# Performance work log

Hardware: AMD Instinct MI355X
Metric: run time of the kernel (lower is better)

The kernel has to match this reference:

```python
import jax, jax.numpy as jnp
import numpy as np

T, B, I, H, L = 512, 64, 1024, 1024, 2


def setup_inputs() -> dict:
    key = jax.random.key(0)
    ks = jax.random.split(key, 3)
    stdv = 1.0 / np.sqrt(H)
    x = jax.random.normal(ks[0], (T, B, I), dtype=jnp.float32)
    w_ih = jax.random.uniform(ks[1], (L, 4 * H, I), dtype=jnp.float32, minval=-stdv, maxval=stdv)
    w_hh = jax.random.uniform(ks[2], (L, 4 * H, H), dtype=jnp.float32, minval=-stdv, maxval=stdv)
    b_ih = jnp.zeros((L, 4 * H), dtype=jnp.float32)
    b_hh = jnp.zeros((L, 4 * H), dtype=jnp.float32)
    h0 = jnp.zeros((L, B, H), dtype=jnp.float32)
    c0 = jnp.zeros((L, B, H), dtype=jnp.float32)
    return {"x": x, "h0": h0, "c0": c0, "w_ih": w_ih, "w_hh": w_hh, "b_ih": b_ih, "b_hh": b_hh}


def _lstm_layer(seq, h, c, w_ih_l, w_hh_l, b_ih_l, b_hh_l):
    # in2hidden: one big GEMM over all timesteps, as in the torch code
    igates = jnp.einsum('tbi,gi->tbg', seq, w_ih_l) + b_ih_l  # (T, B, 4H)

    def step(carry, ig):
        h, c = carry
        gates = ig + h @ w_hh_l.T + b_hh_l          # (B, 4H)
        i_g, f_g, g_g, o_g = jnp.split(gates, 4, axis=-1)
        c = jax.nn.sigmoid(f_g) * c + jax.nn.sigmoid(i_g) * jnp.tanh(g_g)
        h = jax.nn.sigmoid(o_g) * jnp.tanh(c)
        return (h, c), h

    (hT, cT), out = jax.lax.scan(step, (h, c), igates)
    return out, hT, cT


def reference(x, h0, c0, w_ih, w_hh, b_ih, b_hh):
    out = x
    h_fin, c_fin = [], []
    for l in range(L):  # small fixed number of structurally distinct layers
        out, hT, cT = _lstm_layer(out, h0[l], c0[l], w_ih[l], w_hh[l], b_ih[l], b_hh[l])
        h_fin.append(hT)
        c_fin.append(cT)
    return out, jnp.stack(h_fin), jnp.stack(c_fin)
```

## Files before the change

### kernel.cpp

```cpp
#include <hip/hip_runtime.h>
#include <hip/hip_bf16.h>
#include <stdint.h>

#define T_STEPS 512
#define NBATCH 64
#define HID 1024
#define NGATE 4096
#define NLAYERS 2
#define BH (NBATCH * HID)
#define TBH (T_STEPS * NBATCH * HID)
#define WEL ((size_t)NLAYERS * NGATE * HID)
#define GBLK 128

typedef __attribute__((ext_vector_type(8))) short short8;
typedef __attribute__((ext_vector_type(4))) float f32x4;

__device__ __forceinline__ ushort f2bf(float f) {
  union { float f; uint32_t i; } u; u.f = f;
  return (ushort)((u.i + 0x7fffu + ((u.i >> 16) & 1u)) >> 16);
}
__device__ __forceinline__ void gll16(const void* g, void* l) {
  __builtin_amdgcn_global_load_lds(
      (const __attribute__((address_space(1))) unsigned int*)g,
      (__attribute__((address_space(3))) unsigned int*)l, 16, 0, 0);
}

#define ISSC(S, P, OFF) \
  asm volatile("global_load_dwordx4 %0, %1, off offset:" #OFF \
               : "=v"(fr[S]) : "v"(P));
#define VMW(N, SLOT) \
  asm volatile("s_waitcnt vmcnt(" #N ")" : "+v"(fr[SLOT]));
#define CON(SLOT, KC) { \
    const short8 b0v = *(const short8*)(bb0 + ((((KC) * 64) + kb) ^ bsw)); \
    const short8 b1v = *(const short8*)(bb1 + ((((KC) * 64) + kb) ^ bsw)); \
    accA = __builtin_amdgcn_mfma_f32_16x16x32_bf16(fr[SLOT], b0v, accA, 0, 0, 0); \
    accB = __builtin_amdgcn_mfma_f32_16x16x32_bf16(fr[SLOT], b1v, accB, 0, 0, 0); }

#define PIPE64() \
  ISSC(0,A0p,0)    ISSC(1,A0p,64)   ISSC(2,A0p,128)  ISSC(3,A0p,192)  \
  ISSC(4,A0p,256)  ISSC(5,A0p,320)  ISSC(6,A0p,384)  ISSC(7,A0p,448)  \
  ISSC(8,A0p,512)  ISSC(9,A0p,576)  ISSC(10,A0p,640) ISSC(11,A0p,704) \
  ISSC(12,A0p,768) ISSC(13,A0p,832) ISSC(14,A0p,896) ISSC(15,A0p,960) \
  VMW(15,0)  CON(0,0)   ISSC(0,A0p,1024)  \
  VMW(15,1)  CON(1,1)   ISSC(1,A0p,1088)  \
  VMW(15,2)  CON(2,2)   ISSC(2,A0p,1152)  \
  VMW(15,3)  CON(3,3)   ISSC(3,A0p,1216)  \
  VMW(15,4)  CON(4,4)   ISSC(4,A0p,1280)  \
  VMW(15,5)  CON(5,5)   ISSC(5,A0p,1344)  \
  VMW(15,6)  CON(6,6)   ISSC(6,A0p,1408)  \
  VMW(15,7)  CON(7,7)   ISSC(7,A0p,1472)  \
  VMW(15,8)  CON(8,8)   ISSC(8,A0p,1536)  \
  VMW(15,9)  CON(9,9)   ISSC(9,A0p,1600)  \
  VMW(15,10) CON(10,10) ISSC(10,A0p,1664) \
  VMW(15,11) CON(11,11) ISSC(11,A0p,1728) \
  VMW(15,12) CON(12,12) ISSC(12,A0p,1792) \
  VMW(15,13) CON(13,13) ISSC(13,A0p,1856) \
  VMW(15,14) CON(14,14) ISSC(14,A0p,1920) \
  VMW(15,15) CON(15,15) ISSC(15,A0p,1984) \
  VMW(15,0)  CON(0,16)  ISSC(0,A1p,0)     \
  VMW(15,1)  CON(1,17)  ISSC(1,A1p,64)    \
  VMW(15,2)  CON(2,18)  ISSC(2,A1p,128)   \
  VMW(15,3)  CON(3,19)  ISSC(3,A1p,192)   \
  VMW(15,4)  CON(4,20)  ISSC(4,A1p,256)   \
  VMW(15,5)  CON(5,21)  ISSC(5,A1p,320)   \
  VMW(15,6)  CON(6,22)  ISSC(6,A1p,384)   \
  VMW(15,7)  CON(7,23)  ISSC(7,A1p,448)   \
  VMW(15,8)  CON(8,24)  ISSC(8,A1p,512)   \
  VMW(15,9)  CON(9,25)  ISSC(9,A1p,576)   \
  VMW(15,10) CON(10,26) ISSC(10,A1p,640)  \
  VMW(15,11) CON(11,27) ISSC(11,A1p,704)  \
  VMW(15,12) CON(12,28) ISSC(12,A1p,768)  \
  VMW(15,13) CON(13,29) ISSC(13,A1p,832)  \
  VMW(15,14) CON(14,30) ISSC(14,A1p,896)  \
  VMW(15,15) CON(15,31) ISSC(15,A1p,960)  \
  VMW(15,0)  CON(0,32)  ISSC(0,A1p,1024)  \
  VMW(15,1)  CON(1,33)  ISSC(1,A1p,1088)  \
  VMW(15,2)  CON(2,34)  ISSC(2,A1p,1152)  \
  VMW(15,3)  CON(3,35)  ISSC(3,A1p,1216)  \
  VMW(15,4)  CON(4,36)  ISSC(4,A1p,1280)  \
  VMW(15,5)  CON(5,37)  ISSC(5,A1p,1344)  \
  VMW(15,6)  CON(6,38)  ISSC(6,A1p,1408)  \
  VMW(15,7)  CON(7,39)  ISSC(7,A1p,1472)  \
  VMW(15,8)  CON(8,40)  ISSC(8,A1p,1536)  \
  VMW(15,9)  CON(9,41)  ISSC(9,A1p,1600)  \
  VMW(15,10) CON(10,42) ISSC(10,A1p,1664) \
  VMW(15,11) CON(11,43) ISSC(11,A1p,1728) \
  VMW(15,12) CON(12,44) ISSC(12,A1p,1792) \
  VMW(15,13) CON(13,45) ISSC(13,A1p,1856) \
  VMW(15,14) CON(14,46) ISSC(14,A1p,1920) \
  VMW(15,15) CON(15,47) ISSC(15,A1p,1984) \
  VMW(15,0)  CON(0,48)  \
  VMW(14,1)  CON(1,49)  \
  VMW(13,2)  CON(2,50)  \
  VMW(12,3)  CON(3,51)  \
  VMW(11,4)  CON(4,52)  \
  VMW(10,5)  CON(5,53)  \
  VMW(9,6)   CON(6,54)  \
  VMW(8,7)   CON(7,55)  \
  VMW(7,8)   CON(8,56)  \
  VMW(6,9)   CON(9,57)  \
  VMW(5,10)  CON(10,58) \
  VMW(4,11)  CON(11,59) \
  VMW(3,12)  CON(12,60) \
  VMW(2,13)  CON(13,61) \
  VMW(1,14)  CON(14,62) \
  VMW(0,15)  CON(15,63)

__global__ void k_f32_to_bf16(const float* __restrict__ in, ushort* __restrict__ out, int n) {
  int i = (blockIdx.x * blockDim.x + threadIdx.x) * 4;
  if (i >= n) return;
  const float4 v = *reinterpret_cast<const float4*>(in + i);
  ushort4 o; o.x = f2bf(v.x); o.y = f2bf(v.y); o.z = f2bf(v.z); o.w = f2bf(v.w);
  *reinterpret_cast<ushort4*>(out + i) = o;
}
__global__ void k_zero(int* p, int n) {
  int i = blockIdx.x * blockDim.x + threadIdx.x;
  if (i < n) p[i] = 0;
}

struct ScanP {
  const ushort* wih; const ushort* whh;
  const ushort* xb;  const ushort* hinit;
  ushort* h0r;
  ushort* h1r;
  const float* c0; const float* bi; const float* bh;
  float* out; int* bar;
};

__device__ __forceinline__ void gbar(int* gb, int phase, int stripe, bool isRoot) {
  __syncthreads();
  if (threadIdx.x == 0) {
    __hip_atomic_fetch_add(gb + stripe * 16, 1, __ATOMIC_RELAXED, __HIP_MEMORY_SCOPE_AGENT);
    if (isRoot) {
      const int target = (phase + 1) * GBLK;
      for (;;) {
        int sum = 0;
#pragma unroll
        for (int i = 0; i < 16; ++i)
          sum += __hip_atomic_load(gb + i * 16, __ATOMIC_RELAXED, __HIP_MEMORY_SCOPE_AGENT);
        if (sum >= target) break;
        __builtin_amdgcn_s_sleep(1);
      }
      __hip_atomic_store(gb + 256, phase + 1, __ATOMIC_RELAXED, __HIP_MEMORY_SCOPE_AGENT);
    } else {
      while (__hip_atomic_load(gb + 256, __ATOMIC_RELAXED, __HIP_MEMORY_SCOPE_AGENT) < phase + 1)
        __builtin_amdgcn_s_sleep(2);
    }
  }
  __syncthreads();
  __builtin_amdgcn_sched_barrier(0);
}

__global__ __launch_bounds__(256, 1) void k_scan(ScanP p) {
  __shared__ __align__(16) ushort Wl[32 * 2048];
  __shared__ float glds[64 * 33];
  const int tid = threadIdx.x, wave = tid >> 6, lane = tid & 63;
  const bool isL1 = blockIdx.x >= 128;
  const int cb = isL1 ? (int)blockIdx.x - 128 : (int)blockIdx.x;
  const int j0 = cb * 8;
  const int stripe = cb & 15;
  const bool isRoot = (cb == 0);
  int* gb = p.bar + (isL1 ? 512 : 0);
  int* rel0 = p.bar + 256;

  const ushort* wihL = p.wih + (isL1 ? (size_t)NGATE * HID : 0);
  const ushort* whhL = p.whh + (isL1 ? (size_t)NGATE * HID : 0);
  for (int q = wave; q < 128; q += 4) {
    const int i = q >> 2, ch = q & 3;
    const ushort* base = (ch < 2) ? wihL : whhL;
    const int g = (i >> 3) * 1024 + j0 + (i & 7);
    gll16(base + (size_t)g * 1024 + (ch & 1) * 512 + (((lane * 16) ^ ((i & 7) << 4)) >> 1),
          (char*)Wl + i * 4096 + ch * 1024);
  }

  const int eb  = tid >> 2;
  const int jl0 = (tid & 3) * 2;
  const int jj  = j0 + jl0;
  const int lofs = isL1 ? NGATE : 0;
  float creg[2], bias[4][2];
#pragma unroll
  for (int i = 0; i < 2; ++i) creg[i] = p.c0[(isL1 ? BH : 0) + eb * 1024 + jj + i];
#pragma unroll
  for (int g = 0; g < 4; ++g)
#pragma unroll
    for (int i = 0; i < 2; ++i)
      bias[g][i] = p.bi[lofs + g * 1024 + jj + i] + p.bh[lofs + g * 1024 + jj + i];

  const size_t aoff = (size_t)(wave * 16 + (lane & 15)) * 1024 + (size_t)((lane >> 4) * 8);
  const int r0 = lane & 15;
  const char* bb0 = (const char*)Wl + r0 * 4096;
  const char* bb1 = (const char*)Wl + (r0 + 16) * 4096;
  const int bsw = (r0 & 7) << 4;
  const int kb = (lane >> 4) * 16;

  __syncthreads();

  for (int t = 0; t < T_STEPS; ++t) {
    if (isL1) {
      if (threadIdx.x == 0) {
        while (__hip_atomic_load(rel0, __ATOMIC_RELAXED, __HIP_MEMORY_SCOPE_AGENT) < t + 1)
          __builtin_amdgcn_s_sleep(2);
      }
      __syncthreads();
      __builtin_amdgcn_sched_barrier(0);
    }

    f32x4 accA = {0.f, 0.f, 0.f, 0.f}, accB = {0.f, 0.f, 0.f, 0.f};
    short8 fr[16];
    {
      const ushort* A0p;
      const ushort* A1p;
      if (!isL1) {
        A0p = p.xb + (size_t)t * BH + aoff;
        A1p = ((t == 0) ? p.hinit : p.h0r + (size_t)(t - 1) * BH) + aoff;
      } else {
        A0p = p.h0r + (size_t)t * BH + aoff;
        A1p = ((t == 0) ? p.hinit + BH : p.h1r + (size_t)(t - 1) * BH) + aoff;
      }
      PIPE64()
    }
#pragma unroll
    for (int r = 0; r < 4; ++r) {
      const int row = wave * 16 + (lane >> 4) * 4 + r;
      glds[row * 33 + r0]      = accA[r];
      glds[row * 33 + 16 + r0] = accB[r];
    }
    __syncthreads();

    float hres[2];
#pragma unroll
    for (int i = 0; i < 2; ++i) {
      const int jl = jl0 + i;
      const float gi = glds[eb * 33 + jl]      + bias[0][i];
      const float gf = glds[eb * 33 + 8 + jl]  + bias[1][i];
      const float gg = glds[eb * 33 + 16 + jl] + bias[2][i];
      const float go = glds[eb * 33 + 24 + jl] + bias[3][i];
      float c = creg[i];
      const float si = 1.f / (1.f + __expf(-gi));
      const float sf = 1.f / (1.f + __expf(-gf));
      const float so = 1.f / (1.f + __expf(-go));
      const float tg = tanhf(gg);
      c = sf * c + si * tg;
      hres[i] = so * tanhf(c);
      creg[i] = c;
    }

    const uint32_t packed = (uint32_t)f2bf(hres[0]) | ((uint32_t)f2bf(hres[1]) << 16);
    ushort* hdst = (!isL1) ? (p.h0r + (size_t)t * BH) : (p.h1r + (size_t)t * BH);
    uint32_t* hw = (uint32_t*)(hdst + eb * 1024 + jj);
    __hip_atomic_store(hw, packed, __ATOMIC_RELAXED, __HIP_MEMORY_SCOPE_AGENT);
    uint32_t chk = __hip_atomic_load(hw, __ATOMIC_RELAXED, __HIP_MEMORY_SCOPE_AGENT);
    asm volatile("" :: "v"(chk));

    if (isL1) {
#pragma unroll
      for (int i = 0; i < 2; ++i)
        p.out[(size_t)t * BH + eb * 1024 + jj + i] = hres[i];
      if (t == T_STEPS - 1) {
#pragma unroll
        for (int i = 0; i < 2; ++i) {
          p.out[(size_t)TBH + BH + eb * 1024 + jj + i] = hres[i];
          p.out[(size_t)TBH + 3 * BH + eb * 1024 + jj + i] = creg[i];
        }
      }
    } else if (t == T_STEPS - 1) {
#pragma unroll
      for (int i = 0; i < 2; ++i) {
        p.out[(size_t)TBH + eb * 1024 + jj + i] = hres[i];
        p.out[(size_t)TBH + 2 * BH + eb * 1024 + jj + i] = creg[i];
      }
    }

    gbar(gb, t, stripe, isRoot);
  }
}

extern "C" void kernel_launch(void* const* d_in, const int* in_sizes, int n_in,
                              void* d_out, int out_size, void* d_ws, size_t ws_size,
                              hipStream_t stream) {
  const float* x    = (const float*)d_in[0];
  const float* h0   = (const float*)d_in[1];
  const float* c0   = (const float*)d_in[2];
  const float* w_ih = (const float*)d_in[3];
  const float* w_hh = (const float*)d_in[4];
  const float* b_ih = (const float*)d_in[5];
  const float* b_hh = (const float*)d_in[6];
  float* out = (float*)d_out;

  ushort* xb    = (ushort*)d_ws;
  ushort* wihb  = xb + (size_t)TBH;
  ushort* whhb  = wihb + WEL;
  ushort* hinit = whhb + WEL;
  ushort* h0r   = hinit + 2 * (size_t)BH;
  ushort* h1r   = h0r + (size_t)TBH;
  int*    bar   = (int*)(h1r + (size_t)TBH);

  const size_t need = ((size_t)3 * TBH + 2 * WEL + 2 * (size_t)BH) * 2 + 4096;
  if (ws_size < need) return;

  { int n = TBH;        k_f32_to_bf16<<<(n / 4 + 255) / 256, 256, 0, stream>>>(x, xb, n); }
  { int n = (int)WEL;   k_f32_to_bf16<<<(n / 4 + 255) / 256, 256, 0, stream>>>(w_ih, wihb, n); }
  { int n = (int)WEL;   k_f32_to_bf16<<<(n / 4 + 255) / 256, 256, 0, stream>>>(w_hh, whhb, n); }
  { int n = 2 * BH;     k_f32_to_bf16<<<(n / 4 + 255) / 256, 256, 0, stream>>>(h0, hinit, n); }
  k_zero<<<4, 256, 0, stream>>>(bar, 1024);

  ScanP sp;
  sp.wih = wihb; sp.whh = whhb;
  sp.xb = xb; sp.hinit = hinit;
  sp.h0r = h0r; sp.h1r = h1r;
  sp.c0 = c0; sp.bi = b_ih; sp.bh = b_hh;
  sp.out = out; sp.bar = bar;

  void* kp[1] = {&sp};
  hipLaunchCooperativeKernel(reinterpret_cast<void*>(&k_scan),
                             dim3(256), dim3(256), kp, 0, stream);
}
```

Baseline: 6.001 ms.

## Split grid barrier into arrive/wait and overlap input-half GEMM with barrier wait

The per-step global barrier is split into an arrive at the end of a step and a wait placed mid-step. Each block first runs the half of the gate GEMM that does not depend on the previous step's hidden state (x for layer 0, layer-0 output for layer 1), then waits, then runs the recurrent half. This hides barrier latency behind useful MFMA work. Layer-1 blocks also cache the last observed release counter to skip redundant polling, and layer 0's root performs one final release after the loop. Risk: the pipeline now drains twice per step, and the memory ordering of h writes relies on relaxed atomics placed after __syncthreads.

```diff
diff --git a/kernel.cpp b/kernel.cpp
--- a/kernel.cpp
+++ b/kernel.cpp
@@ -36,75 +36,43 @@
     accA = __builtin_amdgcn_mfma_f32_16x16x32_bf16(fr[SLOT], b0v, accA, 0, 0, 0); \
     accB = __builtin_amdgcn_mfma_f32_16x16x32_bf16(fr[SLOT], b1v, accB, 0, 0, 0); }
 
-#define PIPE64() \
-  ISSC(0,A0p,0)    ISSC(1,A0p,64)   ISSC(2,A0p,128)  ISSC(3,A0p,192)  \
-  ISSC(4,A0p,256)  ISSC(5,A0p,320)  ISSC(6,A0p,384)  ISSC(7,A0p,448)  \
-  ISSC(8,A0p,512)  ISSC(9,A0p,576)  ISSC(10,A0p,640) ISSC(11,A0p,704) \
-  ISSC(12,A0p,768) ISSC(13,A0p,832) ISSC(14,A0p,896) ISSC(15,A0p,960) \
-  VMW(15,0)  CON(0,0)   ISSC(0,A0p,1024)  \
-  VMW(15,1)  CON(1,1)   ISSC(1,A0p,1088)  \
-  VMW(15,2)  CON(2,2)   ISSC(2,A0p,1152)  \
-  VMW(15,3)  CON(3,3)   ISSC(3,A0p,1216)  \
-  VMW(15,4)  CON(4,4)   ISSC(4,A0p,1280)  \
-  VMW(15,5)  CON(5,5)   ISSC(5,A0p,1344)  \
-  VMW(15,6)  CON(6,6)   ISSC(6,A0p,1408)  \
-  VMW(15,7)  CON(7,7)   ISSC(7,A0p,1472)  \
-  VMW(15,8)  CON(8,8)   ISSC(8,A0p,1536)  \
-  VMW(15,9)  CON(9,9)   ISSC(9,A0p,1600)  \
-  VMW(15,10) CON(10,10) ISSC(10,A0p,1664) \
-  VMW(15,11) CON(11,11) ISSC(11,A0p,1728) \
-  VMW(15,12) CON(12,12) ISSC(12,A0p,1792) \
-  VMW(15,13) CON(13,13) ISSC(13,A0p,1856) \
-  VMW(15,14) CON(14,14) ISSC(14,A0p,1920) \
-  VMW(15,15) CON(15,15) ISSC(15,A0p,1984) \
-  VMW(15,0)  CON(0,16)  ISSC(0,A1p,0)     \
-  VMW(15,1)  CON(1,17)  ISSC(1,A1p,64)    \
-  VMW(15,2)  CON(2,18)  ISSC(2,A1p,128)   \
-  VMW(15,3)  CON(3,19)  ISSC(3,A1p,192)   \
-  VMW(15,4)  CON(4,20)  ISSC(4,A1p,256)   \
-  VMW(15,5)  CON(5,21)  ISSC(5,A1p,320)   \
-  VMW(15,6)  CON(6,22)  ISSC(6,A1p,384)   \
-  VMW(15,7)  CON(7,23)  ISSC(7,A1p,448)   \
-  VMW(15,8)  CON(8,24)  ISSC(8,A1p,512)   \
-  VMW(15,9)  CON(9,25)  ISSC(9,A1p,576)   \
-  VMW(15,10) CON(10,26) ISSC(10,A1p,640)  \
-  VMW(15,11) CON(11,27) ISSC(11,A1p,704)  \
-  VMW(15,12) CON(12,28) ISSC(12,A1p,768)  \
-  VMW(15,13) CON(13,29) ISSC(13,A1p,832)  \
-  VMW(15,14) CON(14,30) ISSC(14,A1p,896)  \
-  VMW(15,15) CON(15,31) ISSC(15,A1p,960)  \
-  VMW(15,0)  CON(0,32)  ISSC(0,A1p,1024)  \
-  VMW(15,1)  CON(1,33)  ISSC(1,A1p,1088)  \
-  VMW(15,2)  CON(2,34)  ISSC(2,A1p,1152)  \
-  VMW(15,3)  CON(3,35)  ISSC(3,A1p,1216)  \
-  VMW(15,4)  CON(4,36)  ISSC(4,A1p,1280)  \
-  VMW(15,5)  CON(5,37)  ISSC(5,A1p,1344)  \
-  VMW(15,6)  CON(6,38)  ISSC(6,A1p,1408)  \
-  VMW(15,7)  CON(7,39)  ISSC(7,A1p,1472)  \
-  VMW(15,8)  CON(8,40)  ISSC(8,A1p,1536)  \
-  VMW(15,9)  CON(9,41)  ISSC(9,A1p,1600)  \
-  VMW(15,10) CON(10,42) ISSC(10,A1p,1664) \
-  VMW(15,11) CON(11,43) ISSC(11,A1p,1728) \
-  VMW(15,12) CON(12,44) ISSC(12,A1p,1792) \
-  VMW(15,13) CON(13,45) ISSC(13,A1p,1856) \
-  VMW(15,14) CON(14,46) ISSC(14,A1p,1920) \
-  VMW(15,15) CON(15,47) ISSC(15,A1p,1984) \
-  VMW(15,0)  CON(0,48)  \
-  VMW(14,1)  CON(1,49)  \
-  VMW(13,2)  CON(2,50)  \
-  VMW(12,3)  CON(3,51)  \
-  VMW(11,4)  CON(4,52)  \
-  VMW(10,5)  CON(5,53)  \
-  VMW(9,6)   CON(6,54)  \
-  VMW(8,7)   CON(7,55)  \
-  VMW(7,8)   CON(8,56)  \
-  VMW(6,9)   CON(9,57)  \
-  VMW(5,10)  CON(10,58) \
-  VMW(4,11)  CON(11,59) \
-  VMW(3,12)  CON(12,60) \
-  VMW(2,13)  CON(13,61) \
-  VMW(1,14)  CON(14,62) \
-  VMW(0,15)  CON(15,63)
+#define PIPE32(Pp, KB) \
+  ISSC(0,Pp,0)    ISSC(1,Pp,64)   ISSC(2,Pp,128)  ISSC(3,Pp,192)  \
+  ISSC(4,Pp,256)  ISSC(5,Pp,320)  ISSC(6,Pp,384)  ISSC(7,Pp,448)  \
+  ISSC(8,Pp,512)  ISSC(9,Pp,576)  ISSC(10,Pp,640) ISSC(11,Pp,704) \
+  ISSC(12,Pp,768) ISSC(13,Pp,832) ISSC(14,Pp,896) ISSC(15,Pp,960) \
+  VMW(15,0)  CON(0,(KB)+0)   ISSC(0,Pp,1024)  \
+  VMW(15,1)  CON(1,(KB)+1)   ISSC(1,Pp,1088)  \
+  VMW(15,2)  CON(2,(KB)+2)   ISSC(2,Pp,1152)  \
+  VMW(15,3)  CON(3,(KB)+3)   ISSC(3,Pp,1216)  \
+  VMW(15,4)  CON(4,(KB)+4)   ISSC(4,Pp,1280)  \
+  VMW(15,5)  CON(5,(KB)+5)   ISSC(5,Pp,1344)  \
+  VMW(15,6)  CON(6,(KB)+6)   ISSC(6,Pp,1408)  \
+  VMW(15,7)  CON(7,(KB)+7)   ISSC(7,Pp,1472)  \
+  VMW(15,8)  CON(8,(KB)+8)   ISSC(8,Pp,1536)  \
+  VMW(15,9)  CON(9,(KB)+9)   ISSC(9,Pp,1600)  \
+  VMW(15,10) CON(10,(KB)+10) ISSC(10,Pp,1664) \
+  VMW(15,11) CON(11,(KB)+11) ISSC(11,Pp,1728) \
+  VMW(15,12) CON(12,(KB)+12) ISSC(12,Pp,1792) \
+  VMW(15,13) CON(13,(KB)+13) ISSC(13,Pp,1856) \
+  VMW(15,14) CON(14,(KB)+14) ISSC(14,Pp,1920) \
+  VMW(15,15) CON(15,(KB)+15) ISSC(15,Pp,1984) \
+  VMW(15,0)  CON(0,(KB)+16)  \
+  VMW(14,1)  CON(1,(KB)+17)  \
+  VMW(13,2)  CON(2,(KB)+18)  \
+  VMW(12,3)  CON(3,(KB)+19)  \
+  VMW(11,4)  CON(4,(KB)+20)  \
+  VMW(10,5)  CON(5,(KB)+21)  \
+  VMW(9,6)   CON(6,(KB)+22)  \
+  VMW(8,7)   CON(7,(KB)+23)  \
+  VMW(7,8)   CON(8,(KB)+24)  \
+  VMW(6,9)   CON(9,(KB)+25)  \
+  VMW(5,10)  CON(10,(KB)+26) \
+  VMW(4,11)  CON(11,(KB)+27) \
+  VMW(3,12)  CON(12,(KB)+28) \
+  VMW(2,13)  CON(13,(KB)+29) \
+  VMW(1,14)  CON(14,(KB)+30) \
+  VMW(0,15)  CON(15,(KB)+31)
 
 __global__ void k_f32_to_bf16(const float* __restrict__ in, ushort* __restrict__ out, int n) {
   int i = (blockIdx.x * blockDim.x + threadIdx.x) * 4;
@@ -127,23 +95,26 @@
   float* out; int* bar;
 };
 
-__device__ __forceinline__ void gbar(int* gb, int phase, int stripe, bool isRoot) {
+__device__ __forceinline__ void garrive(int* gb, int stripe) {
   __syncthreads();
+  if (threadIdx.x == 0)
+    __hip_atomic_fetch_add(gb + stripe * 16, 1, __ATOMIC_RELAXED, __HIP_MEMORY_SCOPE_AGENT);
+}
+__device__ __forceinline__ void gwait(int* gb, int target, bool isRoot) {
   if (threadIdx.x == 0) {
-    __hip_atomic_fetch_add(gb + stripe * 16, 1, __ATOMIC_RELAXED, __HIP_MEMORY_SCOPE_AGENT);
     if (isRoot) {
-      const int target = (phase + 1) * GBLK;
+      const int need = target * GBLK;
       for (;;) {
         int sum = 0;
 #pragma unroll
         for (int i = 0; i < 16; ++i)
           sum += __hip_atomic_load(gb + i * 16, __ATOMIC_RELAXED, __HIP_MEMORY_SCOPE_AGENT);
-        if (sum >= target) break;
+        if (sum >= need) break;
         __builtin_amdgcn_s_sleep(1);
       }
-      __hip_atomic_store(gb + 256, phase + 1, __ATOMIC_RELAXED, __HIP_MEMORY_SCOPE_AGENT);
+      __hip_atomic_store(gb + 256, target, __ATOMIC_RELAXED, __HIP_MEMORY_SCOPE_AGENT);
     } else {
-      while (__hip_atomic_load(gb + 256, __ATOMIC_RELAXED, __HIP_MEMORY_SCOPE_AGENT) < phase + 1)
+      while (__hip_atomic_load(gb + 256, __ATOMIC_RELAXED, __HIP_MEMORY_SCOPE_AGENT) < target)
         __builtin_amdgcn_s_sleep(2);
     }
   }
@@ -193,32 +164,40 @@
   const int bsw = (r0 & 7) << 4;
   const int kb = (lane >> 4) * 16;
 
+  int seen0 = 0;
+
   __syncthreads();
 
   for (int t = 0; t < T_STEPS; ++t) {
-    if (isL1) {
-      if (threadIdx.x == 0) {
-        while (__hip_atomic_load(rel0, __ATOMIC_RELAXED, __HIP_MEMORY_SCOPE_AGENT) < t + 1)
+    f32x4 accA = {0.f, 0.f, 0.f, 0.f}, accB = {0.f, 0.f, 0.f, 0.f};
+    short8 fr[16];
+
+    if (!isL1) {
+      { const ushort* Pp = p.xb + (size_t)t * BH + aoff;
+        PIPE32(Pp, 0) }
+      if (t > 0) gwait(gb, t, isRoot);
+      { const ushort* Qp = ((t == 0) ? p.hinit
+                                     : p.h0r + (size_t)(t - 1) * BH) + aoff;
+        PIPE32(Qp, 32) }
+    } else {
+      if (threadIdx.x == 0 && seen0 < t + 1) {
+        int v = __hip_atomic_load(rel0, __ATOMIC_RELAXED, __HIP_MEMORY_SCOPE_AGENT);
+        while (v < t + 1) {
           __builtin_amdgcn_s_sleep(2);
+          v = __hip_atomic_load(rel0, __ATOMIC_RELAXED, __HIP_MEMORY_SCOPE_AGENT);
+        }
+        seen0 = v;
       }
       __syncthreads();
       __builtin_amdgcn_sched_barrier(0);
-    }
-
-    f32x4 accA = {0.f, 0.f, 0.f, 0.f}, accB = {0.f, 0.f, 0.f, 0.f};
-    short8 fr[16];
-    {
-      const ushort* A0p;
-      const ushort* A1p;
-      if (!isL1) {
-        A0p = p.xb + (size_t)t * BH + aoff;
-        A1p = ((t == 0) ? p.hinit : p.h0r + (size_t)(t - 1) * BH) + aoff;
-      } else {
-        A0p = p.h0r + (size_t)t * BH + aoff;
-        A1p = ((t == 0) ? p.hinit + BH : p.h1r + (size_t)(t - 1) * BH) + aoff;
-      }
-      PIPE64()
-    }
+      { const ushort* Pp = p.h0r + (size_t)t * BH + aoff;
+        PIPE32(Pp, 0) }
+      if (t > 0) gwait(gb, t, isRoot);
+      { const ushort* Qp = ((t == 0) ? p.hinit + BH
+                                     : p.h1r + (size_t)(t - 1) * BH) + aoff;
+        PIPE32(Qp, 32) }
+    }
+
 #pragma unroll
     for (int r = 0; r < 4; ++r) {
       const int row = wave * 16 + (lane >> 4) * 4 + r;
@@ -271,7 +250,20 @@
       }
     }
 
-    gbar(gb, t, stripe, isRoot);
+    garrive(gb, stripe);
+  }
+
+  if (!isL1 && isRoot && threadIdx.x == 0) {
+    const int need = T_STEPS * GBLK;
+    for (;;) {
+      int sum = 0;
+#pragma unroll
+      for (int i = 0; i < 16; ++i)
+        sum += __hip_atomic_load(gb + i * 16, __ATOMIC_RELAXED, __HIP_MEMORY_SCOPE_AGENT);
+      if (sum >= need) break;
+      __builtin_amdgcn_s_sleep(1);
+    }
+    __hip_atomic_store(gb + 256, T_STEPS + 1, __ATOMIC_RELAXED, __HIP_MEMORY_SCOPE_AGENT);
   }
 }
 
```

Result: faster. 5.552 ms (-7.5%).
